# Optimization experiments

Measured on AMD Instinct MI355X. Metric: run time of the kernel, lower is better.

Reference implementation:

```python
import jax, jax.numpy as jnp
import numpy as np

NEG_INF = -1e30

def setup_inputs() -> dict:
    key = jax.random.key(0)
    kx, kq, kk, kv = jax.random.split(key, 4)
    B, T, C, H = 4, 4096, 2048, 128
    x = jax.random.normal(kx, (B, T, C), dtype=jnp.float32)
    Wq = jax.random.normal(kq, (C, H), dtype=jnp.float32) * (C ** -0.5)
    Wk = jax.random.normal(kk, (C, H), dtype=jnp.float32) * (C ** -0.5)
    Wv = jax.random.normal(kv, (C, H), dtype=jnp.float32) * (C ** -0.5)
    return {"x": x, "Wq": Wq, "Wk": Wk, "Wv": Wv}

def reference(x, Wq, Wk, Wv):
    B, T, C = x.shape
    q = x @ Wq  # [B, T, H]
    k = x @ Wk
    v = x @ Wv
    # NOTE: original scales by channels**-0.5 (n_embd), not head_size**-0.5
    scale = C ** -0.5
    wei = jnp.einsum('bqh,bkh->bqk', q, k) * scale  # [B, T, T]
    causal = jnp.tril(jnp.ones((T, T), dtype=bool))
    wei = jnp.where(causal, wei, NEG_INF)
    wei = jax.nn.softmax(wei, axis=-1)
    return jnp.einsum('bqk,bkh->bqh', wei, v)
```

## Files before the change

### kernel.cpp

```cpp
#include <hip/hip_runtime.h>


typedef __attribute__((ext_vector_type(8))) short s8v;
typedef __attribute__((ext_vector_type(4))) float f4v;

__device__ __forceinline__ unsigned short f2bf(float f) {
  unsigned int b = __float_as_uint(f);
  b += 0x7FFFu + ((b >> 16) & 1u);
  return (unsigned short)(b >> 16);
}
__device__ __forceinline__ unsigned int pk2bf(float lo, float hi) {
  return (unsigned int)f2bf(lo) | ((unsigned int)f2bf(hi) << 16);
}

#define SCALE_QK 0.02209708691207961f

__global__ void prep_wt(const float* __restrict__ Wq, const float* __restrict__ Wk,
                        const float* __restrict__ Wv, unsigned short* __restrict__ WT) {
  int e = blockIdx.x * 256 + threadIdx.x;
  int m = e >> 18;
  int r = e & 262143;
  int c = r >> 7, h = r & 127;
  const float* W = (m == 0) ? Wq : (m == 1) ? Wk : Wv;
  float v = W[r];
  if (m == 0) v *= SCALE_QK;
  WT[m * 262144 + h * 2048 + c] = f2bf(v);
}

__global__ __launch_bounds__(512, 1) void proj_kernel(
    const float* __restrict__ x, const unsigned short* __restrict__ WT,
    unsigned short* __restrict__ Qo, unsigned short* __restrict__ Ko,
    unsigned short* __restrict__ VTo)
{
  __shared__ __align__(16) char psmem[116736];
  unsigned short* scr = (unsigned short*)psmem;

  const int tid = threadIdx.x;
  const int w = tid >> 6, lane = tid & 63;
  const int l15 = lane & 15, g = lane >> 4;
  const int wr = w >> 2, wc = w & 3;
  const int rowbase = blockIdx.x * 64;

  f4v acc[12];
  #pragma unroll
  for (int n = 0; n < 12; ++n) acc[n] = (f4v){0.f, 0.f, 0.f, 0.f};

  const int arow = tid >> 3;
  const int akc  = (tid & 7) * 16;
  const float* xsrc = x + (size_t)(rowbase + arow) * 2048 + (tid & 7) * 8;
  const char* WTb = (const char*)WT;

#define STAGE_B(dst_, k0_)                                                     \
  {                                                                            \
    _Pragma("unroll")                                                          \
    for (int p = 0; p < 6; ++p) {                                              \
      const int off = tid * 16 + p * 8192;                                     \
      const int row = off >> 7, chunk = off & 127;                             \
      __builtin_amdgcn_global_load_lds(                                        \
        (const __attribute__((address_space(1))) void*)(                       \
            WTb + (size_t)row * 4096 + (size_t)(k0_) * 2 +                     \
            (chunk ^ ((row & 7) << 4))),                                       \
        (__attribute__((address_space(3))) void*)((dst_) + off), 16, 0, 0);    \
    }                                                                          \
  }

#define WRITE_A(dst_, aa_, ab_)                                                \
  {                                                                            \
    s8v t_;                                                                    \
    _Pragma("unroll")                                                          \
    for (int i = 0; i < 4; ++i) { t_[i] = (short)f2bf(aa_[i]);                 \
                                  t_[i + 4] = (short)f2bf(ab_[i]); }           \
    *(s8v*)((dst_) + arow * 144 + akc) = t_;                                   \
  }

#define COMPUTE(SEL)                                                           \
  {                                                                            \
    const char* Bb = psmem + (SEL) * 49152;                                    \
    const char* Ab = psmem + 98304 + (SEL) * 9216;                             \
    s8v af[2][2], bfr[6][2];                                                   \
    _Pragma("unroll")                                                          \
    for (int mi = 0; mi < 2; ++mi)                                             \
      _Pragma("unroll")                                                        \
      for (int kk = 0; kk < 2; ++kk)                                           \
        af[mi][kk] = *(const s8v*)(Ab + (32 * wr + 16 * mi + l15) * 144 +      \
                                   kk * 64 + g * 16);                          \
    _Pragma("unroll")                                                          \
    for (int nl = 0; nl < 6; ++nl) {                                           \
      const int row = 96 * wc + 16 * nl + l15;                                 \
      _Pragma("unroll")                                                        \
      for (int kk = 0; kk < 2; ++kk)                                           \
        bfr[nl][kk] = *(const s8v*)(Bb + row * 128 +                           \
                       ((kk * 64 + g * 16) ^ ((l15 & 7) << 4)));               \
    }                                                                          \
    __builtin_amdgcn_s_setprio(1);                                             \
    _Pragma("unroll")                                                          \
    for (int kk = 0; kk < 2; ++kk)                                             \
      _Pragma("unroll")                                                        \
      for (int mi = 0; mi < 2; ++mi)                                           \
        _Pragma("unroll")                                                      \
        for (int nl = 0; nl < 6; ++nl)                                         \
          acc[mi * 6 + nl] = __builtin_amdgcn_mfma_f32_16x16x32_bf16(          \
              af[mi][kk], bfr[nl][kk], acc[mi * 6 + nl], 0, 0, 0);             \
    __builtin_amdgcn_s_setprio(0);                                             \
  }

  f4v xa0a = *(const f4v*)(xsrc);
  f4v xa0b = *(const f4v*)(xsrc + 4);
  f4v xa1a = *(const f4v*)(xsrc + 64);
  f4v xa1b = *(const f4v*)(xsrc + 68);
  STAGE_B(psmem, 0)
  WRITE_A(psmem + 98304, xa0a, xa0b)
  xa0a = *(const f4v*)(xsrc + 128);
  xa0b = *(const f4v*)(xsrc + 132);
  __syncthreads();

  for (int k0 = 0; k0 < 2048; k0 += 128) {
    {
      STAGE_B(psmem + 49152, k0 + 64)
      WRITE_A(psmem + 107520, xa1a, xa1b)
      if (k0 + 192 < 2048) {
        xa1a = *(const f4v*)(xsrc + k0 + 192);
        xa1b = *(const f4v*)(xsrc + k0 + 196);
      }
      COMPUTE(0)
      __syncthreads();
    }
    {
      if (k0 + 128 < 2048) {
        STAGE_B(psmem, k0 + 128)
        WRITE_A(psmem + 98304, xa0a, xa0b)
        if (k0 + 256 < 2048) {
          xa0a = *(const f4v*)(xsrc + k0 + 256);
          xa0b = *(const f4v*)(xsrc + k0 + 260);
        }
      }
      COMPUTE(1)
      __syncthreads();
    }
  }
#undef STAGE_B
#undef WRITE_A
#undef COMPUTE

  #pragma unroll
  for (int mi = 0; mi < 2; ++mi) {
    #pragma unroll
    for (int nl = 0; nl < 6; ++nl) {
      const int colg = 96 * wc + 16 * nl + l15;
      const int m = colg >> 7;
      const int h = colg & 127;
      const f4v a = acc[mi * 6 + nl];
      if (m < 2) {
        unsigned short* dst = (m == 0) ? Qo : Ko;
        #pragma unroll
        for (int r = 0; r < 4; ++r) {
          const int t = rowbase + 32 * wr + 16 * mi + 4 * g + r;
          dst[(size_t)t * 128 + h] = f2bf(a[r]);
        }
      } else {
        #pragma unroll
        for (int r = 0; r < 4; ++r) {
          const int tl = 32 * wr + 16 * mi + 4 * g + r;
          scr[h * 72 + tl] = f2bf(a[r]);
        }
      }
    }
  }
  __syncthreads();
  {
    const int b   = rowbase >> 12;
    const int tg0 = rowbase & 4095;
    const int h    = tid >> 2;
    const int toff = (tid & 3) * 16;
    unsigned short* dst = VTo + (size_t)(b * 128 + h) * 4096 + tg0 + toff;
    *(s8v*)(dst)     = *(const s8v*)(&scr[h * 72 + toff]);
    *(s8v*)(dst + 8) = *(const s8v*)(&scr[h * 72 + toff + 8]);
  }
}

__global__ __launch_bounds__(256, 2) void attn_kernel(
    const unsigned short* __restrict__ Q, const unsigned short* __restrict__ K,
    const unsigned short* __restrict__ VT, float* __restrict__ out)
{
  __shared__ __align__(16) char smem[71168];
  unsigned short* plds = (unsigned short*)(smem + 65536);
  float* mlp = (float*)(smem + 70656);

  const int tid  = threadIdx.x;
  const int w    = tid >> 6;
  const int lane = tid & 63;
  const int l15 = lane & 15, g = lane >> 4;

  const int b  = blockIdx.x & 3;
  const int s  = 127 - (blockIdx.x >> 2);
  const int qb = s * 32;
  const int roff = (w >> 1) * 16, half = w & 1;
  const int ntiles = (qb + 95) >> 6;

  const char* Kg = (const char*)(K  + (size_t)b * 4096 * 128);
  const char* Vg = (const char*)(VT + (size_t)b * 128 * 4096);
  const unsigned short* Qb = Q + (size_t)b * 4096 * 128;

  s8v qf[4];
  #pragma unroll
  for (int kk = 0; kk < 4; ++kk)
    qf[kk] = *(const s8v*)(Qb + (size_t)(qb + roff + l15) * 128 + kk * 32 + g * 8);

  f4v o[8];
  #pragma unroll
  for (int n = 0; n < 8; ++n) o[n] = (f4v){0.f, 0.f, 0.f, 0.f};
  float mrun = -1e30f, lrun = 0.f;

  const int off0 = tid * 16;

#define STAGE(Kl_, kvb_)                                                       \
  {                                                                            \
    char* Kl = (Kl_);                                                          \
    _Pragma("unroll")                                                          \
    for (int p = 0; p < 4; ++p) {                                              \
      const int off = off0 + p * 4096;                                         \
      const int ks = off ^ (((off >> 8) & 7) << 4);                            \
      __builtin_amdgcn_global_load_lds(                                        \
        (const __attribute__((address_space(1))) void*)(Kg + (size_t)(kvb_) * 256 + ks), \
        (__attribute__((address_space(3))) void*)(Kl + off), 16, 0, 0);        \
    }                                                                          \
    _Pragma("unroll")                                                          \
    for (int p = 0; p < 4; ++p) {                                              \
      const int off = off0 + p * 4096;                                         \
      const int h = off >> 7;                                                  \
      const int cs = (off & 127) ^ ((h & 7) << 4);                             \
      __builtin_amdgcn_global_load_lds(                                        \
        (const __attribute__((address_space(1))) void*)(Vg + (size_t)h * 8192 + (size_t)(kvb_) * 2 + cs), \
        (__attribute__((address_space(3))) void*)(Kl + 16384 + off), 16, 0, 0); \
    }                                                                          \
  }

  STAGE(smem, 0)
  __syncthreads();

  int cur = 0;
  for (int it = 0; it < ntiles; ++it) {
    const int kvb = it * 64;
    if (it + 1 < ntiles) STAGE(smem + (cur ^ 1) * 32768, kvb + 64)

    const char* Kl = smem + cur * 32768;
    const char* Vl = Kl + 16384;
    s8v kf[2][4];
    #pragma unroll
    for (int t2 = 0; t2 < 2; ++t2) {
      const int row = half * 32 + t2 * 16 + l15;
      #pragma unroll
      for (int kk = 0; kk < 4; ++kk)
        kf[t2][kk] = *(const s8v*)(Kl + ((row * 256 + kk * 64 + g * 16) ^ ((l15 & 7) << 4)));
    }
    s8v vf[8];
    #pragma unroll
    for (int n = 0; n < 8; ++n) {
      const int row = n * 16 + l15;
      vf[n] = *(const s8v*)(Vl + ((row * 128 + half * 64 + g * 16) ^ ((l15 & 7) << 4)));
    }
    f4v sc[2];
    sc[0] = (f4v){0.f, 0.f, 0.f, 0.f};
    sc[1] = (f4v){0.f, 0.f, 0.f, 0.f};
    __builtin_amdgcn_s_setprio(1);
    #pragma unroll
    for (int kk = 0; kk < 4; ++kk) {
      sc[0] = __builtin_amdgcn_mfma_f32_16x16x32_bf16(kf[0][kk], qf[kk], sc[0], 0, 0, 0);
      sc[1] = __builtin_amdgcn_mfma_f32_16x16x32_bf16(kf[1][kk], qf[kk], sc[1], 0, 0, 0);
    }
    __builtin_amdgcn_s_setprio(0);
    if (it == ntiles - 1) {
      const int qrow = qb + roff + l15;
      #pragma unroll
      for (int t2 = 0; t2 < 2; ++t2)
        #pragma unroll
        for (int r = 0; r < 4; ++r) {
          const int kv = kvb + half * 32 + 16 * t2 + 4 * g + r;
          if (kv > qrow) sc[t2][r] = -1e30f;
        }
    }
    float v = fmaxf(fmaxf(fmaxf(sc[0][0], sc[0][1]), fmaxf(sc[0][2], sc[0][3])),
                    fmaxf(fmaxf(sc[1][0], sc[1][1]), fmaxf(sc[1][2], sc[1][3])));
    v = fmaxf(v, __shfl_xor(v, 16));
    v = fmaxf(v, __shfl_xor(v, 32));
    if (__any(v > mrun + 4.0f)) {
      const float mnew = fmaxf(mrun, v);
      const float corr = __expf(mrun - mnew);
      mrun = mnew;
      lrun *= corr;
      #pragma unroll
      for (int n = 0; n < 8; ++n)
        #pragma unroll
        for (int r = 0; r < 4; ++r) o[n][r] *= corr;
    }
    f4v p0, p1;
    #pragma unroll
    for (int r = 0; r < 4; ++r) {
      p0[r] = __expf(sc[0][r] - mrun);
      p1[r] = __expf(sc[1][r] - mrun);
    }
    lrun += (p0[0] + p0[1]) + (p0[2] + p0[3]) + (p1[0] + p1[1]) + (p1[2] + p1[3]);
    unsigned short* pw = plds + w * 640;
    *(unsigned int*)(&pw[l15 * 40 + 4 * g])          = pk2bf(p0[0], p0[1]);
    *(unsigned int*)(&pw[l15 * 40 + 4 * g + 2])      = pk2bf(p0[2], p0[3]);
    *(unsigned int*)(&pw[l15 * 40 + 16 + 4 * g])     = pk2bf(p1[0], p1[1]);
    *(unsigned int*)(&pw[l15 * 40 + 16 + 4 * g + 2]) = pk2bf(p1[2], p1[3]);
    const s8v pf = *(const s8v*)(pw + l15 * 40 + g * 8);
    __builtin_amdgcn_s_setprio(1);
    #pragma unroll
    for (int n = 0; n < 8; ++n)
      o[n] = __builtin_amdgcn_mfma_f32_16x16x32_bf16(vf[n], pf, o[n], 0, 0, 0);
    __builtin_amdgcn_s_setprio(0);

    __syncthreads();
    cur ^= 1;
  }
#undef STAGE

  float lt = lrun;
  lt += __shfl_xor(lt, 16);
  lt += __shfl_xor(lt, 32);
  if (g == 0) {
    mlp[(w * 16 + l15) * 2 + 0] = mrun;
    mlp[(w * 16 + l15) * 2 + 1] = lt;
  }
  float* ol = (float*)smem;
  #pragma unroll
  for (int n = 0; n < 8; ++n)
    *(f4v*)(&ol[(w * 16 + l15) * 132 + 16 * n + 4 * g]) = o[n];
  __syncthreads();

  {
    const int st  = tid >> 7;
    const int t7  = tid & 127;
    const int row = t7 >> 3;
    const int hb  = (t7 & 7) * 16;
    const int wA = 2 * st, wB = 2 * st + 1;
    const float m0 = mlp[(wA * 16 + row) * 2], l0 = mlp[(wA * 16 + row) * 2 + 1];
    const float m1 = mlp[(wB * 16 + row) * 2], l1 = mlp[(wB * 16 + row) * 2 + 1];
    const float M  = fmaxf(m0, m1);
    const float w0 = __expf(m0 - M), w1 = __expf(m1 - M);
    const float inv = 1.0f / (w0 * l0 + w1 * l1);
    float* dst = out + (size_t)(b * 4096 + qb + 16 * st + row) * 128 + hb;
    #pragma unroll
    for (int j4 = 0; j4 < 4; ++j4) {
      const f4v a = *(const f4v*)(&ol[(wA * 16 + row) * 132 + hb + 4 * j4]);
      const f4v c = *(const f4v*)(&ol[(wB * 16 + row) * 132 + hb + 4 * j4]);
      f4v res;
      #pragma unroll
      for (int j = 0; j < 4; ++j) res[j] = (w0 * a[j] + w1 * c[j]) * inv;
      *(f4v*)(dst + 4 * j4) = res;
    }
  }
}

extern "C" void kernel_launch(void* const* d_in, const int* in_sizes, int n_in,
                              void* d_out, int out_size, void* d_ws, size_t ws_size,
                              hipStream_t stream) {
  const float* x  = (const float*)d_in[0];
  const float* Wq = (const float*)d_in[1];
  const float* Wk = (const float*)d_in[2];
  const float* Wv = (const float*)d_in[3];

  unsigned short* WT = (unsigned short*)d_ws;
  unsigned short* Q  = (unsigned short*)((char*)d_ws + 1572864);
  unsigned short* K  = (unsigned short*)((char*)d_ws + 5767168);
  unsigned short* VT = (unsigned short*)((char*)d_ws + 9961472);
  float* out = (float*)d_out;

  prep_wt<<<3072, 256, 0, stream>>>(Wq, Wk, Wv, WT);
  proj_kernel<<<256, 512, 0, stream>>>(x, WT, Q, K, VT);
  attn_kernel<<<512, 256, 0, stream>>>(Q, K, VT, out);
}
```

Before: 119.7 us.

## Restructure projection GEMM pipeline with explicit waitcnt barriers and reorder attention blocks

The projection GEMM main loop is rewritten as a macro-driven double-buffered pipeline. It uses explicit s_waitcnt on lgkmcnt and vmcnt, raw s_barrier and sched_barrier fences, and a peeled tail, replacing __syncthreads. This lets outstanding global loads for x stay in flight across the barrier instead of draining everything each step. The attention kernel's block-to-query-tile mapping also changes: the first 256 blocks take the heaviest tiles in descending order and the rest take tiles in ascending order, which changes load balance across the causal triangle. Hand-set vmcnt values risk wrong synchronization if the number of in-flight loads differs from what is assumed.

```diff
diff --git a/kernel.cpp b/kernel.cpp
--- a/kernel.cpp
+++ b/kernel.cpp
@@ -104,40 +104,50 @@
     __builtin_amdgcn_s_setprio(0);                                             \
   }
 
-  f4v xa0a = *(const f4v*)(xsrc);
-  f4v xa0b = *(const f4v*)(xsrc + 4);
-  f4v xa1a = *(const f4v*)(xsrc + 64);
-  f4v xa1b = *(const f4v*)(xsrc + 68);
+#define PBODY(SEL, K0, XA, XB, DOX, WN)                                        \
+  {                                                                            \
+    if ((K0) + 64 < 2048) {                                                    \
+      STAGE_B(psmem + ((SEL) ^ 1) * 49152, (K0) + 64)                          \
+    }                                                                          \
+    __builtin_amdgcn_sched_barrier(0);      \
+    if ((K0) + 64 < 2048) {                                                    \
+      WRITE_A(psmem + 98304 + ((SEL) ^ 1) * 9216, XA, XB)                      \
+    }                                                                          \
+    if (DOX) {                                                                 \
+      XA = *(const f4v*)(xsrc + (K0) + 192);                                   \
+      XB = *(const f4v*)(xsrc + (K0) + 196);                                   \
+    }                                                                          \
+    COMPUTE(SEL)                                                               \
+    asm volatile("s_waitcnt lgkmcnt(0)" ::: "memory");                         \
+    asm volatile("s_waitcnt vmcnt(" #WN ")" ::: "memory");                     \
+    __builtin_amdgcn_s_barrier();                                              \
+    __builtin_amdgcn_sched_barrier(0);                                         \
+  }
+
+  f4v xe_a = *(const f4v*)(xsrc);
+  f4v xe_b = *(const f4v*)(xsrc + 4);
   STAGE_B(psmem, 0)
-  WRITE_A(psmem + 98304, xa0a, xa0b)
-  xa0a = *(const f4v*)(xsrc + 128);
-  xa0b = *(const f4v*)(xsrc + 132);
-  __syncthreads();
-
-  for (int k0 = 0; k0 < 2048; k0 += 128) {
-    {
-      STAGE_B(psmem + 49152, k0 + 64)
-      WRITE_A(psmem + 107520, xa1a, xa1b)
-      if (k0 + 192 < 2048) {
-        xa1a = *(const f4v*)(xsrc + k0 + 192);
-        xa1b = *(const f4v*)(xsrc + k0 + 196);
-      }
-      COMPUTE(0)
-      __syncthreads();
-    }
-    {
-      if (k0 + 128 < 2048) {
-        STAGE_B(psmem, k0 + 128)
-        WRITE_A(psmem + 98304, xa0a, xa0b)
-        if (k0 + 256 < 2048) {
-          xa0a = *(const f4v*)(xsrc + k0 + 256);
-          xa0b = *(const f4v*)(xsrc + k0 + 260);
-        }
-      }
-      COMPUTE(1)
-      __syncthreads();
-    }
-  }
+  __builtin_amdgcn_sched_barrier(0);
+  f4v xo_a = *(const f4v*)(xsrc + 64);
+  f4v xo_b = *(const f4v*)(xsrc + 68);
+  WRITE_A(psmem + 98304, xe_a, xe_b)
+  xe_a = *(const f4v*)(xsrc + 128);
+  xe_b = *(const f4v*)(xsrc + 132);
+  asm volatile("s_waitcnt lgkmcnt(0)" ::: "memory");
+  asm volatile("s_waitcnt vmcnt(4)" ::: "memory");
+  __builtin_amdgcn_s_barrier();
+  __builtin_amdgcn_sched_barrier(0);
+
+  for (int it = 0; it < 14; ++it) {
+    const int k0 = it * 128;
+    PBODY(0, k0, xo_a, xo_b, 1, 2)
+    PBODY(1, k0 + 64, xe_a, xe_b, 1, 2)
+  }
+  PBODY(0, 1792, xo_a, xo_b, 1, 2)
+  PBODY(1, 1856, xe_a, xe_b, 0, 0)
+  PBODY(0, 1920, xo_a, xo_b, 0, 0)
+  COMPUTE(1)
+#undef PBODY
 #undef STAGE_B
 #undef WRITE_A
 #undef COMPUTE
@@ -191,8 +201,11 @@
   const int lane = tid & 63;
   const int l15 = lane & 15, g = lane >> 4;
 
-  const int b  = blockIdx.x & 3;
-  const int s  = 127 - (blockIdx.x >> 2);
+  const int bid = blockIdx.x;
+  const int i8  = bid & 255;
+  const int j   = i8 >> 2;
+  const int s   = (bid < 256) ? (127 - j) : j;
+  const int b   = i8 & 3;
   const int qb = s * 32;
   const int roff = (w >> 1) * 16, half = w & 1;
   const int ntiles = (qb + 95) >> 6;
@@ -348,7 +361,7 @@
       const f4v c = *(const f4v*)(&ol[(wB * 16 + row) * 132 + hb + 4 * j4]);
       f4v res;
       #pragma unroll
-      for (int j = 0; j < 4; ++j) res[j] = (w0 * a[j] + w1 * c[j]) * inv;
+      for (int jj = 0; jj < 4; ++jj) res[jj] = (w0 * a[jj] + w1 * c[jj]) * inv;
       *(f4v*)(dst + 4 * j4) = res;
     }
   }
```

New measurement: 111.3 us. 7.0% less time.
